# Kernel tuning notes

Hardware: AMD Instinct MI355X
Metric: run time of the kernel (lower is better)

Reference implementation:

```python
import jax, jax.numpy as jnp
import numpy as np

N_NUC = 100_000
N_NN = 1_600_000
EMB = 128
MSG = 32
OUT = 128
LN_EPS = 1e-6  # flax LayerNorm default


def setup_inputs() -> dict:
    key = jax.random.key(0)
    ks = jax.random.split(key, 12)
    inp = {
        "s_embed": jax.random.normal(ks[0], (N_NUC, EMB), jnp.float32),
        "r_embed": jax.random.normal(ks[1], (N_NUC, EMB), jnp.float32),
        "e_embed": jax.random.normal(ks[2], (N_NN, MSG), jnp.float32),
        "norm": jax.random.uniform(ks[3], (N_NUC,), jnp.float32),
        "senders": jax.random.randint(ks[4], (N_NN,), 0, N_NUC, jnp.int32),
        "receivers": jax.random.randint(ks[5], (N_NN,), 0, N_NUC, jnp.int32),
        # learned parameters
        "W_s": jax.random.normal(ks[6], (EMB, MSG), jnp.float32) / np.sqrt(EMB),
        "b_s": jnp.zeros((MSG,), jnp.float32),
        "W_r": jax.random.normal(ks[7], (EMB, MSG), jnp.float32) / np.sqrt(EMB),
        "b_r": jnp.zeros((MSG,), jnp.float32),
        "ln_scale": jnp.ones((MSG,), jnp.float32),
        "ln_bias": jnp.zeros((MSG,), jnp.float32),
        "W_e": jax.random.normal(ks[8], (MSG, MSG), jnp.float32) / np.sqrt(MSG),
        "W_out": jax.random.normal(ks[9], (MSG, OUT), jnp.float32) / np.sqrt(MSG),
    }
    return inp


def _layernorm(x, scale, bias):
    mu = jnp.mean(x, axis=-1, keepdims=True)
    var = jnp.mean(jnp.square(x - mu), axis=-1, keepdims=True)
    return (x - mu) * jax.lax.rsqrt(var + LN_EPS) * scale + bias


def reference(s_embed, r_embed, e_embed, norm, senders, receivers,
              W_s, b_s, W_r, b_r, ln_scale, ln_bias, W_e, W_out):
    # Dense projections on nodes, then gather per edge: [n_nn, msg]
    inp = (s_embed @ W_s + b_s)[senders] + (r_embed @ W_r + b_r)[receivers]
    inp = _layernorm(inp, ln_scale, ln_bias)
    inp = jax.nn.silu(inp)
    inp = inp * (e_embed @ W_e)  # elementwise edge gating
    # scatter-add to receivers: [n_nuc, msg]
    msg = jax.ops.segment_sum(inp, receivers, num_segments=s_embed.shape[0])
    msg = msg * norm[:, None]
    return jax.nn.silu(msg @ W_out)
```

## Files before the change

### kernel.cpp

```cpp
#include <hip/hip_runtime.h>
#include <hip/hip_bf16.h>
#include <math.h>

#define N_NUC_C 100000
#define N_NN_C  1600000
#define EMB_C   128
#define MSG_C   32
#define OUT_C   128
#define NB1     98
#define NPART   8
#define R_PER_P (N_NUC_C / NPART)
#define SBLK    784
#define STHREADS (SBLK * 256)
#define LDS_USTR 17
#define RANK_BLOCKS 6250
#define PROJ_BLOCKS 1564

typedef __attribute__((ext_vector_type(8))) short bf16x8;
typedef __attribute__((ext_vector_type(4))) float f32x4;

__device__ __forceinline__ float silu_f(float y) {
    return y / (1.0f + __expf(-y));
}

__device__ __forceinline__ unsigned pack_bf16x2(float a, float b) {
    unsigned ua = __float_as_uint(a); ua += 0x7FFFu + ((ua >> 16) & 1u);
    unsigned ub = __float_as_uint(b); ub += 0x7FFFu + ((ub >> 16) & 1u);
    return (ua >> 16) | (ub & 0xFFFF0000u);
}

__device__ __forceinline__ unsigned short bf16_of(float a) {
    unsigned ua = __float_as_uint(a); ua += 0x7FFFu + ((ua >> 16) & 1u);
    return (unsigned short)(ua >> 16);
}

__device__ __forceinline__ void proj_body(
    int n, int pr, int c0,
    const float* __restrict__ s_embed, const float* __restrict__ r_embed,
    const float* __restrict__ W_s, const float* __restrict__ b_s,
    const float* __restrict__ W_r, const float* __restrict__ b_r,
    float* __restrict__ proj)
{
    const float* __restrict__ src = pr ? r_embed : s_embed;
    const float* __restrict__ W   = pr ? W_r : W_s;
    const float* __restrict__ b   = pr ? b_r : b_s;
    float* __restrict__ dst = proj + (size_t)pr * N_NUC_C * MSG_C;

    float acc[16];
    #pragma unroll
    for (int i = 0; i < 16; ++i) acc[i] = b[c0 + i];

    const float* row = src + (size_t)n * EMB_C;
    #pragma unroll 4
    for (int k = 0; k < EMB_C; k += 4) {
        const float4 rv = *reinterpret_cast<const float4*>(row + k);
        #pragma unroll
        for (int i = 0; i < 16; ++i) {
            acc[i] = fmaf(rv.x, W[(k + 0) * MSG_C + c0 + i], acc[i]);
            acc[i] = fmaf(rv.y, W[(k + 1) * MSG_C + c0 + i], acc[i]);
            acc[i] = fmaf(rv.z, W[(k + 2) * MSG_C + c0 + i], acc[i]);
            acc[i] = fmaf(rv.w, W[(k + 3) * MSG_C + c0 + i], acc[i]);
        }
    }

    float4* d = reinterpret_cast<float4*>(dst + (size_t)n * MSG_C + c0);
    d[0] = make_float4(acc[0],  acc[1],  acc[2],  acc[3]);
    d[1] = make_float4(acc[4],  acc[5],  acc[6],  acc[7]);
    d[2] = make_float4(acc[8],  acc[9],  acc[10], acc[11]);
    d[3] = make_float4(acc[12], acc[13], acc[14], acc[15]);
}

__global__ __launch_bounds__(256) void proj_rank_kernel(
    const float* __restrict__ s_embed, const float* __restrict__ r_embed,
    const float* __restrict__ W_s, const float* __restrict__ b_s,
    const float* __restrict__ W_r, const float* __restrict__ b_r,
    float* __restrict__ proj,
    const int* __restrict__ receivers, int* __restrict__ cnt,
    int* __restrict__ rank)
{
    const int bid = blockIdx.x;
    if (bid < RANK_BLOCKS) {
        const int e = bid * 256 + threadIdx.x;
        if (e < N_NN_C) rank[e] = atomicAdd(&cnt[receivers[e]], 1);
        return;
    }
    const int pb  = bid - RANK_BLOCKS;
    const int sub = pb & 3;
    const int n   = (pb >> 2) * 256 + threadIdx.x;
    if (n >= N_NUC_C) return;
    proj_body(n, sub >> 1, (sub & 1) * 16,
              s_embed, r_embed, W_s, b_s, W_r, b_r, proj);
}

__global__ __launch_bounds__(256) void proj_kernel(
    const float* __restrict__ s_embed, const float* __restrict__ r_embed,
    const float* __restrict__ W_s, const float* __restrict__ b_s,
    const float* __restrict__ W_r, const float* __restrict__ b_r,
    float* __restrict__ proj)
{
    const int n = blockIdx.x * blockDim.x + threadIdx.x;
    if (n >= N_NUC_C) return;
    const int sub = blockIdx.y;
    proj_body(n, sub >> 1, (sub & 1) * 16,
              s_embed, r_embed, W_s, b_s, W_r, b_r, proj);
}

__global__ __launch_bounds__(256) void scan1_kernel(
    const int* __restrict__ cnt, int* __restrict__ excl, int* __restrict__ blockTot)
{
    __shared__ int waveTot[4];
    const int t = threadIdx.x, b = blockIdx.x;
    const int lane = t & 63, wid = t >> 6;
    const int base = b * 1024 + t * 4;

    int d0 = (base + 0 < N_NUC_C) ? cnt[base + 0] : 0;
    int d1 = (base + 1 < N_NUC_C) ? cnt[base + 1] : 0;
    int d2 = (base + 2 < N_NUC_C) ? cnt[base + 2] : 0;
    int d3 = (base + 3 < N_NUC_C) ? cnt[base + 3] : 0;
    const int s = d0 + d1 + d2 + d3;

    int incl = s;
    #pragma unroll
    for (int off = 1; off < 64; off <<= 1) {
        int v = __shfl_up(incl, off);
        if (lane >= off) incl += v;
    }
    const int wexcl = incl - s;
    if (lane == 63) waveTot[wid] = incl;
    __syncthreads();
    int wbase = 0;
    for (int w = 0; w < wid; ++w) wbase += waveTot[w];
    const int e0 = wbase + wexcl;

    if (base + 0 < N_NUC_C) excl[base + 0] = e0;
    if (base + 1 < N_NUC_C) excl[base + 1] = e0 + d0;
    if (base + 2 < N_NUC_C) excl[base + 2] = e0 + d0 + d1;
    if (base + 3 < N_NUC_C) excl[base + 3] = e0 + d0 + d1 + d2;
    if (t == 255) blockTot[b] = wbase + incl;
}

__global__ __launch_bounds__(128) void scan2_kernel(
    const int* __restrict__ blockTot, int* __restrict__ blockOff)
{
    __shared__ int sh[128];
    const int t = threadIdx.x;
    const int v = (t < NB1) ? blockTot[t] : 0;
    sh[t] = v;
    __syncthreads();
    #pragma unroll
    for (int off = 1; off < 128; off <<= 1) {
        int x = 0;
        if (t >= off) x = sh[t - off];
        __syncthreads();
        sh[t] += x;
        __syncthreads();
    }
    if (t < NB1) blockOff[t] = sh[t] - v;
}

__global__ __launch_bounds__(256) void scan3_kernel(
    const int* __restrict__ excl, const int* __restrict__ blockOff,
    int* __restrict__ offsets)
{
    const int n = blockIdx.x * blockDim.x + threadIdx.x;
    if (n < N_NUC_C) offsets[n] = excl[n] + blockOff[n >> 10];
    if (n == 0) offsets[N_NUC_C] = N_NN_C;
}

__global__ __launch_bounds__(256) void scatter_pack8_kernel(
    const int* __restrict__ senders, const int* __restrict__ receivers,
    const int* __restrict__ rank, const int* __restrict__ offsets,
    int4* __restrict__ edge_pack)
{
    const int p    = blockIdx.x & 7;
    const int blk  = blockIdx.x >> 3;
    const int base = blk * 256 + threadIdx.x;
    const int rlo  = p * R_PER_P;
    const int rhi  = rlo + R_PER_P;

    #pragma unroll
    for (int k = 0; k < 8; ++k) {
        const int e = base + k * STHREADS;
        if (e < N_NN_C) {
            const int r = receivers[e];
            if (r >= rlo && r < rhi) {
                const int dst = offsets[r] + rank[e];
                edge_pack[dst] = make_int4(e, senders[e], r, 0);
            }
        }
    }
}

__global__ __launch_bounds__(256) void fused_csr_kernel(
    const float* __restrict__ proj,
    const float* __restrict__ e_embed,
    const int4*  __restrict__ edge_pack,
    const int*   __restrict__ offsets,
    const float* __restrict__ ln_scale,
    const float* __restrict__ ln_bias,
    const float* __restrict__ W_e,
    float*       __restrict__ msg)
{
    __shared__ unsigned lds_ev[256 * LDS_USTR];
    __shared__ unsigned lds_g [256 * LDS_USTR];
    __shared__ int      lds_r[256];
    __shared__ int      lds_e[256];

    const int t    = threadIdx.x;
    const int lane = t & 63;
    const int wb   = t & ~63;
    const int B0   = blockIdx.x * 256;

    const int4 pk = edge_pack[B0 + t];
    const int e = pk.x, s = pk.y, r = pk.z;
    lds_r[t] = r;
    lds_e[t] = e;

    bf16x8 bf0, bf1;
    {
        const int kg = (lane >> 4) * 8;
        const int n0 = lane & 15;
        #pragma unroll
        for (int i = 0; i < 8; ++i) {
            bf0[i] = (short)bf16_of(W_e[(kg + i) * MSG_C + n0]);
            bf1[i] = (short)bf16_of(W_e[(kg + i) * MSG_C + 16 + n0]);
        }
    }

    __syncthreads();

    {
        const int rowb = t >> 3;
        const int sub  = t & 7;
        #pragma unroll
        for (int p = 0; p < 8; ++p) {
            const int i  = p * 32 + rowb;
            const int ei = lds_e[i];
            const float4 v = *reinterpret_cast<const float4*>(
                e_embed + (size_t)ei * MSG_C + sub * 4);
            lds_ev[i * LDS_USTR + sub * 2 + 0] = pack_bf16x2(v.x, v.y);
            lds_ev[i * LDS_USTR + sub * 2 + 1] = pack_bf16x2(v.z, v.w);
        }
    }

    __syncthreads();

    {
        unsigned short* g16 = reinterpret_cast<unsigned short*>(lds_g);
        #pragma unroll
        for (int mt = 0; mt < 4; ++mt) {
            const int arow = wb + mt * 16 + (lane & 15);
            const unsigned* ar = &lds_ev[arow * LDS_USTR + ((lane >> 4) << 2)];
            union { unsigned u[4]; bf16x8 v; } cvt;
            cvt.u[0] = ar[0]; cvt.u[1] = ar[1]; cvt.u[2] = ar[2]; cvt.u[3] = ar[3];
            const bf16x8 af = cvt.v;
            f32x4 z = {0.f, 0.f, 0.f, 0.f};
            const f32x4 a0 = __builtin_amdgcn_mfma_f32_16x16x32_bf16(af, bf0, z, 0, 0, 0);
            const f32x4 a1 = __builtin_amdgcn_mfma_f32_16x16x32_bf16(af, bf1, z, 0, 0, 0);
            const int rbase = wb + mt * 16 + ((lane >> 4) << 2);
            #pragma unroll
            for (int rg = 0; rg < 4; ++rg) {
                g16[(rbase + rg) * (2 * LDS_USTR) + (lane & 15)]      = bf16_of(a0[rg]);
                g16[(rbase + rg) * (2 * LDS_USTR) + 16 + (lane & 15)] = bf16_of(a1[rg]);
            }
        }
    }

    __syncthreads();

    float g[MSG_C];
    {
        const unsigned* gr = &lds_g[t * LDS_USTR];
        #pragma unroll
        for (int j = 0; j < 16; ++j) {
            const unsigned u = gr[j];
            g[2*j]   = __uint_as_float(u << 16);
            g[2*j+1] = __uint_as_float(u & 0xFFFF0000u);
        }
    }

    const float4* ps = reinterpret_cast<const float4*>(proj + (size_t)s * MSG_C);
    const float4* pq = reinterpret_cast<const float4*>(proj + (size_t)(N_NUC_C + r) * MSG_C);
    float x[MSG_C];
    #pragma unroll
    for (int q = 0; q < 8; ++q) {
        const float4 a = ps[q];
        const float4 b = pq[q];
        x[4*q+0] = a.x + b.x; x[4*q+1] = a.y + b.y;
        x[4*q+2] = a.z + b.z; x[4*q+3] = a.w + b.w;
    }

    float mu = 0.0f;
    #pragma unroll
    for (int c = 0; c < MSG_C; ++c) mu += x[c];
    mu *= (1.0f / MSG_C);
    float var = 0.0f;
    #pragma unroll
    for (int c = 0; c < MSG_C; ++c) { const float d = x[c] - mu; var = fmaf(d, d, var); }
    var *= (1.0f / MSG_C);
    const float rs = rsqrtf(var + 1e-6f);

    unsigned* orow = &lds_ev[t * LDS_USTR];
    #pragma unroll
    for (int i = 0; i < 16; ++i) {
        const int c0_ = 2*i, c1_ = 2*i + 1;
        const float y0 = (x[c0_] - mu) * rs * ln_scale[c0_] + ln_bias[c0_];
        const float y1 = (x[c1_] - mu) * rs * ln_scale[c1_] + ln_bias[c1_];
        orow[i] = pack_bf16x2(silu_f(y0) * g[c0_], silu_f(y1) * g[c1_]);
    }

    __syncthreads();

    const int r0 = lds_r[0];
    const int r1 = lds_r[255];
    const int total = (r1 - r0 + 1) << 5;

    for (int p = t; p < total; p += 256) {
        const int n  = r0 + (p >> 5);
        const int ch = p & 31;
        int b  = offsets[n];
        int en = offsets[n + 1];
        const bool interior = (b >= B0) && (en <= B0 + 256);
        if (b < B0) b = B0;
        if (en > B0 + 256) en = B0 + 256;

        const int dw  = ch >> 1;
        const bool hi = (ch & 1);
        float sum = 0.0f;
        for (int q = b - B0; q < en - B0; ++q) {
            const unsigned u = lds_ev[q * LDS_USTR + dw];
            sum += __uint_as_float(hi ? (u & 0xFFFF0000u) : (u << 16));
        }

        float* dst = msg + (size_t)n * MSG_C + ch;
        if (interior)       *dst = sum;
        else if (en > b)    atomicAdd(dst, sum);
    }
}

__global__ __launch_bounds__(256) void edge_kernel(
    const float* __restrict__ proj, const float* __restrict__ e_embed,
    const int* __restrict__ senders, const int* __restrict__ receivers,
    const float* __restrict__ ln_scale, const float* __restrict__ ln_bias,
    const float* __restrict__ W_e, float* __restrict__ msg)
{
    const int e = blockIdx.x * blockDim.x + threadIdx.x;
    if (e >= N_NN_C) return;
    const int s = senders[e];
    const int r = receivers[e];
    const float4* ps = reinterpret_cast<const float4*>(proj + (size_t)s * MSG_C);
    const float4* pq = reinterpret_cast<const float4*>(proj + (size_t)(N_NUC_C + r) * MSG_C);
    float x[MSG_C];
    #pragma unroll
    for (int q = 0; q < 8; ++q) {
        const float4 a = ps[q];
        const float4 b = pq[q];
        x[4*q+0] = a.x + b.x; x[4*q+1] = a.y + b.y;
        x[4*q+2] = a.z + b.z; x[4*q+3] = a.w + b.w;
    }
    float mu = 0.0f;
    #pragma unroll
    for (int c = 0; c < MSG_C; ++c) mu += x[c];
    mu *= (1.0f / MSG_C);
    float var = 0.0f;
    #pragma unroll
    for (int c = 0; c < MSG_C; ++c) { const float d = x[c] - mu; var = fmaf(d, d, var); }
    var *= (1.0f / MSG_C);
    const float rs = rsqrtf(var + 1e-6f);
    #pragma unroll
    for (int c = 0; c < MSG_C; ++c) {
        const float y = (x[c] - mu) * rs * ln_scale[c] + ln_bias[c];
        x[c] = silu_f(y);
    }
    float ev[MSG_C];
    const float4* ee = reinterpret_cast<const float4*>(e_embed + (size_t)e * MSG_C);
    #pragma unroll
    for (int q = 0; q < 8; ++q) {
        const float4 v = ee[q];
        ev[4*q+0] = v.x; ev[4*q+1] = v.y; ev[4*q+2] = v.z; ev[4*q+3] = v.w;
    }
    float g[MSG_C];
    #pragma unroll
    for (int c = 0; c < MSG_C; ++c) g[c] = 0.0f;
    #pragma unroll
    for (int k = 0; k < MSG_C; ++k) {
        const float ek = ev[k];
        #pragma unroll
        for (int c = 0; c < MSG_C; ++c) g[c] = fmaf(ek, W_e[k * MSG_C + c], g[c]);
    }
    float* mrow = msg + (size_t)r * MSG_C;
    #pragma unroll
    for (int c = 0; c < MSG_C; ++c) atomicAdd(mrow + c, x[c] * g[c]);
}

__global__ __launch_bounds__(256) void out_kernel(
    const float* __restrict__ msg, const float* __restrict__ norm,
    const float* __restrict__ W_out, float* __restrict__ out)
{
    const int j     = threadIdx.x & (OUT_C - 1);
    const int local = threadIdx.x >> 7;

    float w[MSG_C];
    #pragma unroll
    for (int k = 0; k < MSG_C; ++k) w[k] = W_out[k * OUT_C + j];

    for (int n = blockIdx.x * 2 + local; n < N_NUC_C; n += gridDim.x * 2) {
        const float4* m4 = reinterpret_cast<const float4*>(msg + (size_t)n * MSG_C);
        float acc = 0.0f;
        #pragma unroll
        for (int q = 0; q < 8; ++q) {
            const float4 mv = m4[q];
            acc = fmaf(mv.x, w[4*q+0], acc);
            acc = fmaf(mv.y, w[4*q+1], acc);
            acc = fmaf(mv.z, w[4*q+2], acc);
            acc = fmaf(mv.w, w[4*q+3], acc);
        }
        acc *= norm[n];
        out[(size_t)n * OUT_C + j] = silu_f(acc);
    }
}

extern "C" void kernel_launch(void* const* d_in, const int* in_sizes, int n_in,
                              void* d_out, int out_size, void* d_ws, size_t ws_size,
                              hipStream_t stream) {
    const float* s_embed   = (const float*)d_in[0];
    const float* r_embed   = (const float*)d_in[1];
    const float* e_embed   = (const float*)d_in[2];
    const float* norm      = (const float*)d_in[3];
    const int*   senders   = (const int*)d_in[4];
    const int*   receivers = (const int*)d_in[5];
    const float* W_s       = (const float*)d_in[6];
    const float* b_s       = (const float*)d_in[7];
    const float* W_r       = (const float*)d_in[8];
    const float* b_r       = (const float*)d_in[9];
    const float* ln_scale  = (const float*)d_in[10];
    const float* ln_bias   = (const float*)d_in[11];
    const float* W_e       = (const float*)d_in[12];
    const float* W_out     = (const float*)d_in[13];
    float* out = (float*)d_out;

    char* ws = (char*)d_ws;
    size_t off = 0;
    auto alloc = [&](size_t bytes) { char* p = ws + off; off += (bytes + 255) & ~(size_t)255; return p; };

    float* proj      = (float*)alloc((size_t)2 * N_NUC_C * MSG_C * 4);
    float* msg       = (float*)alloc((size_t)N_NUC_C * MSG_C * 4);
    const size_t off_min = off;
    int*   cnt       = (int*)  alloc((size_t)N_NUC_C * 4);
    int*   excl      = (int*)  alloc((size_t)N_NUC_C * 4);
    int*   offsets   = (int*)  alloc((size_t)(N_NUC_C + 1) * 4);
    int*   blockTot  = (int*)  alloc(128 * 4);
    int*   blockOff  = (int*)  alloc(128 * 4);
    int*   rank      = (int*)  alloc((size_t)N_NN_C * 4);
    int4*  edge_pack = (int4*) alloc((size_t)N_NN_C * 16);
    const size_t off_full = off;

    if (off_full <= ws_size) {
        hipMemsetAsync(cnt, 0, (size_t)N_NUC_C * 4, stream);
        hipMemsetAsync(msg, 0, (size_t)N_NUC_C * MSG_C * 4, stream);
        proj_rank_kernel<<<RANK_BLOCKS + PROJ_BLOCKS, 256, 0, stream>>>(
            s_embed, r_embed, W_s, b_s, W_r, b_r, proj, receivers, cnt, rank);
        scan1_kernel<<<NB1, 256, 0, stream>>>(cnt, excl, blockTot);
        scan2_kernel<<<1, 128, 0, stream>>>(blockTot, blockOff);
        scan3_kernel<<<(N_NUC_C + 255) / 256, 256, 0, stream>>>(excl, blockOff, offsets);
        scatter_pack8_kernel<<<NPART * SBLK, 256, 0, stream>>>(
            senders, receivers, rank, offsets, edge_pack);
        fused_csr_kernel<<<N_NN_C / 256, 256, 0, stream>>>(
            proj, e_embed, edge_pack, offsets, ln_scale, ln_bias, W_e, msg);
    } else if (off_min <= ws_size) {
        dim3 pgrid((N_NUC_C + 255) / 256, 4);
        proj_kernel<<<pgrid, 256, 0, stream>>>(s_embed, r_embed, W_s, b_s, W_r, b_r, proj);
        hipMemsetAsync(msg, 0, (size_t)N_NUC_C * MSG_C * 4, stream);
        edge_kernel<<<(N_NN_C + 255) / 256, 256, 0, stream>>>(
            proj, e_embed, senders, receivers, ln_scale, ln_bias, W_e, msg);
    }

    out_kernel<<<2048, 256, 0, stream>>>(msg, norm, W_out, out);
}
```

Before: 334.9 us.

## Replace global atomic rank counting with chunked LDS byte histograms

```diff
diff --git a/kernel.cpp b/kernel.cpp
--- a/kernel.cpp
+++ b/kernel.cpp
@@ -13,7 +13,12 @@
 #define SBLK    784
 #define STHREADS (SBLK * 256)
 #define LDS_USTR 17
-#define RANK_BLOCKS 6250
+#define NCH2    256
+#define CH2     (N_NN_C / NCH2)
+#define CH2_IT  ((CH2 + 255) / 256)
+#define HPART   2
+#define HR      (N_NUC_C / HPART)
+#define HIST_BLOCKS (NCH2 * HPART)
 #define PROJ_BLOCKS 1564
 
 typedef __attribute__((ext_vector_type(8))) short bf16x8;
@@ -70,21 +75,48 @@
     d[3] = make_float4(acc[12], acc[13], acc[14], acc[15]);
 }
 
-__global__ __launch_bounds__(256) void proj_rank_kernel(
+__global__ __launch_bounds__(256) void proj_hist2_kernel(
     const float* __restrict__ s_embed, const float* __restrict__ r_embed,
     const float* __restrict__ W_s, const float* __restrict__ b_s,
     const float* __restrict__ W_r, const float* __restrict__ b_r,
     float* __restrict__ proj,
-    const int* __restrict__ receivers, int* __restrict__ cnt,
-    int* __restrict__ rank)
-{
+    const int* __restrict__ receivers,
+    unsigned char* __restrict__ lrank8,
+    unsigned char* __restrict__ cnt2)
+{
+    __shared__ unsigned cl[HR / 4];
     const int bid = blockIdx.x;
-    if (bid < RANK_BLOCKS) {
-        const int e = bid * 256 + threadIdx.x;
-        if (e < N_NN_C) rank[e] = atomicAdd(&cnt[receivers[e]], 1);
+
+    if (bid < HIST_BLOCKS) {
+        const int c   = bid >> 1;
+        const int p   = bid & 1;
+        const int rlo = p * HR;
+
+        for (int i = threadIdx.x; i < HR / 4; i += 256) cl[i] = 0;
+        __syncthreads();
+
+        const int ebase = c * CH2;
+        #pragma unroll 1
+        for (int it = 0; it < CH2_IT; ++it) {
+            const int el = it * 256 + threadIdx.x;
+            if (el < CH2) {
+                const int e  = ebase + el;
+                const int rr = receivers[e] - rlo;
+                if ((unsigned)rr < (unsigned)HR) {
+                    const int sh = (rr & 3) * 8;
+                    const unsigned old = atomicAdd(&cl[rr >> 2], 1u << sh);
+                    lrank8[e] = (unsigned char)((old >> sh) & 0xFFu);
+                }
+            }
+        }
+        __syncthreads();
+
+        unsigned* dst = reinterpret_cast<unsigned*>(cnt2 + (size_t)c * N_NUC_C + rlo);
+        for (int i = threadIdx.x; i < HR / 4; i += 256) dst[i] = cl[i];
         return;
     }
-    const int pb  = bid - RANK_BLOCKS;
+
+    const int pb  = bid - HIST_BLOCKS;
     const int sub = pb & 3;
     const int n   = (pb >> 2) * 256 + threadIdx.x;
     if (n >= N_NUC_C) return;
@@ -103,6 +135,22 @@
     const int sub = blockIdx.y;
     proj_body(n, sub >> 1, (sub & 1) * 16,
               s_embed, r_embed, W_s, b_s, W_r, b_r, proj);
+}
+
+__global__ __launch_bounds__(256) void chunkscan_kernel(
+    unsigned char* __restrict__ cnt2, int* __restrict__ cnt)
+{
+    const int r = blockIdx.x * 256 + threadIdx.x;
+    if (r >= N_NUC_C) return;
+    int s = 0;
+    #pragma unroll 8
+    for (int c = 0; c < NCH2; ++c) {
+        unsigned char* p = cnt2 + (size_t)c * N_NUC_C + r;
+        const int t = *p;
+        *p = (unsigned char)s;
+        s += t;
+    }
+    cnt[r] = s;
 }
 
 __global__ __launch_bounds__(256) void scan1_kernel(
@@ -169,8 +217,9 @@
 
 __global__ __launch_bounds__(256) void scatter_pack8_kernel(
     const int* __restrict__ senders, const int* __restrict__ receivers,
-    const int* __restrict__ rank, const int* __restrict__ offsets,
-    int4* __restrict__ edge_pack)
+    const unsigned char* __restrict__ lrank8,
+    const unsigned char* __restrict__ cnt2,
+    const int* __restrict__ offsets, int4* __restrict__ edge_pack)
 {
     const int p    = blockIdx.x & 7;
     const int blk  = blockIdx.x >> 3;
@@ -184,7 +233,9 @@
         if (e < N_NN_C) {
             const int r = receivers[e];
             if (r >= rlo && r < rhi) {
-                const int dst = offsets[r] + rank[e];
+                const int c   = e / CH2;
+                const int dst = offsets[r] + (int)cnt2[(size_t)c * N_NUC_C + r]
+                                          + (int)lrank8[e];
                 edge_pack[dst] = make_int4(e, senders[e], r, 0);
             }
         }
@@ -451,20 +502,21 @@
     int*   offsets   = (int*)  alloc((size_t)(N_NUC_C + 1) * 4);
     int*   blockTot  = (int*)  alloc(128 * 4);
     int*   blockOff  = (int*)  alloc(128 * 4);
-    int*   rank      = (int*)  alloc((size_t)N_NN_C * 4);
+    unsigned char* lrank8 = (unsigned char*)alloc((size_t)N_NN_C);
+    unsigned char* cnt2   = (unsigned char*)alloc((size_t)NCH2 * N_NUC_C);
     int4*  edge_pack = (int4*) alloc((size_t)N_NN_C * 16);
     const size_t off_full = off;
 
     if (off_full <= ws_size) {
-        hipMemsetAsync(cnt, 0, (size_t)N_NUC_C * 4, stream);
         hipMemsetAsync(msg, 0, (size_t)N_NUC_C * MSG_C * 4, stream);
-        proj_rank_kernel<<<RANK_BLOCKS + PROJ_BLOCKS, 256, 0, stream>>>(
-            s_embed, r_embed, W_s, b_s, W_r, b_r, proj, receivers, cnt, rank);
+        proj_hist2_kernel<<<HIST_BLOCKS + PROJ_BLOCKS, 256, 0, stream>>>(
+            s_embed, r_embed, W_s, b_s, W_r, b_r, proj, receivers, lrank8, cnt2);
+        chunkscan_kernel<<<(N_NUC_C + 255) / 256, 256, 0, stream>>>(cnt2, cnt);
         scan1_kernel<<<NB1, 256, 0, stream>>>(cnt, excl, blockTot);
         scan2_kernel<<<1, 128, 0, stream>>>(blockTot, blockOff);
         scan3_kernel<<<(N_NUC_C + 255) / 256, 256, 0, stream>>>(excl, blockOff, offsets);
         scatter_pack8_kernel<<<NPART * SBLK, 256, 0, stream>>>(
-            senders, receivers, rank, offsets, edge_pack);
+            senders, receivers, lrank8, cnt2, offsets, edge_pack);
         fused_csr_kernel<<<N_NN_C / 256, 256, 0, stream>>>(
             proj, e_embed, edge_pack, offsets, ln_scale, ln_bias, W_e, msg);
     } else if (off_min <= ws_size) {
```

Result: faster. 304.0 us (-9.2%).
